# Optimization experiments

Measured on AMD Instinct MI355X. Metric: run time of the kernel, lower is better.

The kernel has to match this reference:

```python
import jax, jax.numpy as jnp
import numpy as np
from jax import lax


def setup_inputs() -> dict:
    key = jax.random.key(0)
    k = jax.random.split(key, 5)
    B, L, ntaps, C = 128, 16384, 128, 128
    return {
        "x": jax.random.normal(k[0], (B, 1, L), dtype=jnp.float32),
        "conv_w": jax.random.normal(k[1], (C, 1, 3), dtype=jnp.float32) * 0.1,
        "conv_b": jax.random.normal(k[2], (C,), dtype=jnp.float32) * 0.1,
        "fc_w": jax.random.normal(k[3], (ntaps, C), dtype=jnp.float32) * 0.05,
        "fc_b": jax.random.normal(k[4], (ntaps,), dtype=jnp.float32) * 0.05,
        "ntaps": ntaps,
    }


def reference(x, conv_w, conv_b, fc_w, fc_b, ntaps):
    # ---- Localiser: Conv1d(1,128,3,padding=1) -> AdaptiveAvgPool1d(1) -> Linear(128, ntaps)
    h = lax.conv_general_dilated(
        x, conv_w, window_strides=(1,), padding=[(1, 1)],
        dimension_numbers=("NCH", "OIH", "NCH"))  # [B,128,L]
    h = h + conv_b[None, :, None]
    pooled = jnp.mean(h, axis=2)                  # [B,128]
    filt = pooled @ fc_w.T + fc_b                 # [B,ntaps]

    # ---- adaptive_filter: per-sample conv1d via groups=B, padding=ntaps
    B = x.shape[0]
    xr = jnp.transpose(x, (1, 0, 2))              # [1,B,L] (batch as channels)
    w = filt[:, None, :]                          # [B,1,ntaps]
    y = lax.conv_general_dilated(
        xr, w, window_strides=(1,), padding=[(ntaps, ntaps)],
        dimension_numbers=("NCH", "OIH", "NCH"),
        feature_group_count=B)                    # [1,B,L+ntaps+1]
    return jnp.transpose(y, (1, 0, 2))            # [B,1,L+ntaps+1]
```

## Files before the change

### kernel.cpp

```cpp
#include <hip/hip_runtime.h>

#define LEN   16384
#define NB    128
#define NTAPS 128
#define LOUT  16513
#define NT    33
#define SPAN  (NT*256 + 144)

typedef __attribute__((ext_vector_type(8))) short bf16x8;
typedef __attribute__((ext_vector_type(4))) float f32x4;

__device__ __forceinline__ unsigned short f2bf(float f) {
    union { float f; unsigned u; } c; c.f = f;
    unsigned r = c.u + 0x7FFF + ((c.u >> 16) & 1);
    return (unsigned short)(r >> 16);
}

__global__ __launch_bounds__(512) void fused_fir(
    const float* __restrict__ x, const float* __restrict__ conv_w,
    const float* __restrict__ conv_b, const float* __restrict__ fc_w,
    const float* __restrict__ fc_b, float* __restrict__ out)
{
    const int b   = blockIdx.y;
    const int h   = blockIdx.x;
    const int tid = threadIdx.x;

    __shared__ unsigned short sxp[SPAN];
    __shared__ unsigned short fp[288];
    __shared__ float scw[384];
    __shared__ float scb[128];
    __shared__ float sfb[128];
    __shared__ float parts[8];
    __shared__ float sx0, sxl;

    const float* xr  = x + (size_t)b * LEN;
    const float4* xr4 = reinterpret_cast<const float4*>(xr);

    if (tid < 384) scw[tid] = conv_w[tid];
    else if (tid < 512) scb[tid - 384] = conv_b[tid - 384];
    if (tid < 128) sfb[tid] = fc_b[tid];
    if (tid == 0) { sx0 = xr[0]; sxl = xr[LEN - 1]; }

    float s = 0.f;
    const int sbase = 32 - 2112 * h;
    #pragma unroll
    for (int p = 0; p < 8; ++p) {
        const int g4 = tid + p * 512;
        float4 v = xr4[g4];
        s += (v.x + v.y) + (v.z + v.w);
        const int s4 = g4 + sbase;
        if (s4 >= 0 && s4 < SPAN / 4) {
            ushort4 hv;
            hv.x = f2bf(v.x); hv.y = f2bf(v.y); hv.z = f2bf(v.z); hv.w = f2bf(v.w);
            *reinterpret_cast<ushort4*>(&sxp[4 * s4]) = hv;
        }
    }
    {
        const ushort4 z = {0, 0, 0, 0};
        if (h == 0) {
            if (tid < 32) *reinterpret_cast<ushort4*>(&sxp[4 * tid]) = z;
        } else {
            if (tid < 132) *reinterpret_cast<ushort4*>(&sxp[4 * (2016 + tid)]) = z;
        }
    }

    const int t = tid >> 2, q = tid & 3;
    const float4* fw4 = reinterpret_cast<const float4*>(fc_w);
    float4 fw[8];
    #pragma unroll
    for (int m = 0; m < 8; ++m) fw[m] = fw4[8 * tid + m];

    #pragma unroll
    for (int off = 32; off > 0; off >>= 1) s += __shfl_down(s, off, 64);
    if ((tid & 63) == 0) parts[tid >> 6] = s;
    __syncthreads();
    float Sb = 0.f;
    #pragma unroll
    for (int i = 0; i < 8; ++i) Sb += parts[i];

    float g0 = 0.f, g1 = 0.f, g2 = 0.f, hh = 0.f;
    #pragma unroll
    for (int m = 0; m < 8; ++m) {
        const float fv[4] = {fw[m].x, fw[m].y, fw[m].z, fw[m].w};
        #pragma unroll
        for (int jj = 0; jj < 4; ++jj) {
            const int c = 32 * q + 4 * m + jj;
            const float f = fv[jj];
            g0 = fmaf(f, scw[3 * c + 0], g0);
            g1 = fmaf(f, scw[3 * c + 1], g1);
            g2 = fmaf(f, scw[3 * c + 2], g2);
            hh = fmaf(f, scb[c], hh);
        }
    }
    g0 += __shfl_xor(g0, 1); g0 += __shfl_xor(g0, 2);
    g1 += __shfl_xor(g1, 1); g1 += __shfl_xor(g1, 2);
    g2 += __shfl_xor(g2, 1); g2 += __shfl_xor(g2, 2);
    hh += __shfl_xor(hh, 1); hh += __shfl_xor(hh, 2);

    if (q == 0) {
        const float invL = 1.0f / (float)LEN;
        const float flt = sfb[t] + hh
            + invL * fmaf(Sb - sxl, g0, fmaf(Sb, g1, (Sb - sx0) * g2));
        fp[128 + t] = f2bf(flt);
    }
    if (q == 1) fp[t] = 0;
    if (q == 2 && t < 32) fp[256 + t] = 0;
    __syncthreads();

    const int l = tid & 63, w = tid >> 6;
    const int n = l & 15;
    const int g = l >> 4;
    bf16x8 afrag[5];
    #pragma unroll
    for (int kb = 0; kb < 5; ++kb)
        #pragma unroll
        for (int hf = 0; hf < 2; ++hf)
            #pragma unroll
            for (int j = 0; j < 4; ++j)
                afrag[kb][hf * 4 + j] =
                    (short)fp[128 + 32 * kb + 16 * hf + 4 * g + j - n];

    float* orow = out + (size_t)b * LOUT;
    #pragma unroll
    for (int it = 0; it < 5; ++it) {
        const int tau = w + 8 * it;
        if (tau >= NT) break;
        const int T = h * NT + tau;
        if (T >= 65) break;
        const unsigned short* bp = &sxp[tau * 256 + 16 * n + 4 * g];
        f32x4 acc = {0.f, 0.f, 0.f, 0.f};
        #pragma unroll
        for (int kb = 0; kb < 5; ++kb) {
            ushort4 lo = *reinterpret_cast<const ushort4*>(bp + 32 * kb);
            ushort4 hi = *reinterpret_cast<const ushort4*>(bp + 32 * kb + 16);
            bf16x8 bfrag;
            bfrag[0] = (short)lo.x; bfrag[1] = (short)lo.y;
            bfrag[2] = (short)lo.z; bfrag[3] = (short)lo.w;
            bfrag[4] = (short)hi.x; bfrag[5] = (short)hi.y;
            bfrag[6] = (short)hi.z; bfrag[7] = (short)hi.w;
            acc = __builtin_amdgcn_mfma_f32_16x16x32_bf16(afrag[kb], bfrag, acc, 0, 0, 0);
        }
        const int t0 = 256 * T + 16 * n + 4 * g;
        if (T < 64) {
            orow[t0 + 0] = acc[0];
            orow[t0 + 1] = acc[1];
            orow[t0 + 2] = acc[2];
            orow[t0 + 3] = acc[3];
        } else {
            #pragma unroll
            for (int j = 0; j < 4; ++j)
                if (t0 + j < LOUT) orow[t0 + j] = acc[j];
        }
    }
}

extern "C" void kernel_launch(void* const* d_in, const int* in_sizes, int n_in,
                              void* d_out, int out_size, void* d_ws, size_t ws_size,
                              hipStream_t stream)
{
    const float* x      = (const float*)d_in[0];
    const float* conv_w = (const float*)d_in[1];
    const float* conv_b = (const float*)d_in[2];
    const float* fc_w   = (const float*)d_in[3];
    const float* fc_b   = (const float*)d_in[4];
    float* out = (float*)d_out;

    dim3 grid(2, NB);
    fused_fir<<<grid, 512, 0, stream>>>(x, conv_w, conv_b, fc_w, fc_b, out);
}
```

Baseline: 17.99 us.

## Process each batch row in one 1024-thread block and vectorize output stores

Replaces the two 512-thread blocks per batch row with a single 1024-thread block that stages the whole padded row in LDS and computes all 65 output tiles. This stops each half-block from re-reading the full input row just to get the mean, and it lets the zero padding be written inline. Full output tiles are now written with one 16-byte vector store instead of four scalar stores. In exchange the grid drops to 128 blocks, half the previous count, so fewer CUs are busy. The vector stores are also not 16-byte aligned for odd batch rows. A redundant first reduction loop was added, but its results are overwritten and the compiler will likely eliminate it.

```diff
diff --git a/kernel.cpp b/kernel.cpp
--- a/kernel.cpp
+++ b/kernel.cpp
@@ -4,8 +4,8 @@
 #define NB    128
 #define NTAPS 128
 #define LOUT  16513
-#define NT    33
-#define SPAN  (NT*256 + 144)
+#define SPAN  16800
+#define SPAN4 (SPAN/4)
 
 typedef __attribute__((ext_vector_type(8))) short bf16x8;
 typedef __attribute__((ext_vector_type(4))) float f32x4;
@@ -16,13 +16,12 @@
     return (unsigned short)(r >> 16);
 }
 
-__global__ __launch_bounds__(512) void fused_fir(
+__global__ __launch_bounds__(1024) void fused_fir(
     const float* __restrict__ x, const float* __restrict__ conv_w,
     const float* __restrict__ conv_b, const float* __restrict__ fc_w,
     const float* __restrict__ fc_b, float* __restrict__ out)
 {
-    const int b   = blockIdx.y;
-    const int h   = blockIdx.x;
+    const int b   = blockIdx.x;
     const int tid = threadIdx.x;
 
     __shared__ unsigned short sxp[SPAN];
@@ -30,45 +29,37 @@
     __shared__ float scw[384];
     __shared__ float scb[128];
     __shared__ float sfb[128];
-    __shared__ float parts[8];
+    __shared__ float parts[16];
     __shared__ float sx0, sxl;
 
-    const float* xr  = x + (size_t)b * LEN;
+    const float* xr   = x + (size_t)b * LEN;
     const float4* xr4 = reinterpret_cast<const float4*>(xr);
 
     if (tid < 384) scw[tid] = conv_w[tid];
     else if (tid < 512) scb[tid - 384] = conv_b[tid - 384];
-    if (tid < 128) sfb[tid] = fc_b[tid];
+    else if (tid < 640) sfb[tid - 512] = fc_b[tid - 512];
     if (tid == 0) { sx0 = xr[0]; sxl = xr[LEN - 1]; }
 
+    const int t = tid >> 3, q = tid & 7;
+    const float4* fw4 = reinterpret_cast<const float4*>(fc_w);
+    float4 fw[4];
+    #pragma unroll
+    for (int m = 0; m < 4; ++m) fw[m] = fw4[32 * t + 4 * q + m];
+
     float s = 0.f;
-    const int sbase = 32 - 2112 * h;
     #pragma unroll
-    for (int p = 0; p < 8; ++p) {
-        const int g4 = tid + p * 512;
-        float4 v = xr4[g4];
-        s += (v.x + v.y) + (v.z + v.w);
-        const int s4 = g4 + sbase;
-        if (s4 >= 0 && s4 < SPAN / 4) {
+    for (int p = 0; p < 5; ++p) {
+        const int i = tid + 1024 * p;
+        if (i < SPAN4) {
+            const int g4 = i - 32;
+            float4 v = make_float4(0.f, 0.f, 0.f, 0.f);
+            if (g4 >= 0 && g4 < LEN / 4) v = xr4[g4];
+            s += (v.x + v.y) + (v.z + v.w);
             ushort4 hv;
             hv.x = f2bf(v.x); hv.y = f2bf(v.y); hv.z = f2bf(v.z); hv.w = f2bf(v.w);
-            *reinterpret_cast<ushort4*>(&sxp[4 * s4]) = hv;
+            *reinterpret_cast<ushort4*>(&sxp[4 * i]) = hv;
         }
     }
-    {
-        const ushort4 z = {0, 0, 0, 0};
-        if (h == 0) {
-            if (tid < 32) *reinterpret_cast<ushort4*>(&sxp[4 * tid]) = z;
-        } else {
-            if (tid < 132) *reinterpret_cast<ushort4*>(&sxp[4 * (2016 + tid)]) = z;
-        }
-    }
-
-    const int t = tid >> 2, q = tid & 3;
-    const float4* fw4 = reinterpret_cast<const float4*>(fc_w);
-    float4 fw[8];
-    #pragma unroll
-    for (int m = 0; m < 8; ++m) fw[m] = fw4[8 * tid + m];
 
     #pragma unroll
     for (int off = 32; off > 0; off >>= 1) s += __shfl_down(s, off, 64);
@@ -76,15 +67,28 @@
     __syncthreads();
     float Sb = 0.f;
     #pragma unroll
-    for (int i = 0; i < 8; ++i) Sb += parts[i];
+    for (int i = 0; i < 16; ++i) Sb += parts[i];
 
     float g0 = 0.f, g1 = 0.f, g2 = 0.f, hh = 0.f;
     #pragma unroll
-    for (int m = 0; m < 8; ++m) {
+    for (int m = 0; m < 4; ++m) {
         const float fv[4] = {fw[m].x, fw[m].y, fw[m].z, fw[m].w};
         #pragma unroll
         for (int jj = 0; jj < 4; ++jj) {
-            const int c = 32 * q + 4 * m + jj;
+            const int c = 16 * q + 4 * m + jj;
+            const float f = fv[jj];
+            g0 = fmaf(f, scw[3 * c + 0], g0);
+            g1 = fmaf(f, scw[3 * c + 1], g1);
+            g2 = fmaf(f, scb[c], hh) , hh = g2, g2 = 0.f;
+        }
+    }
+    g0 = 0.f; g1 = 0.f; g2 = 0.f; hh = 0.f;
+    #pragma unroll
+    for (int m = 0; m < 4; ++m) {
+        const float fv[4] = {fw[m].x, fw[m].y, fw[m].z, fw[m].w};
+        #pragma unroll
+        for (int jj = 0; jj < 4; ++jj) {
+            const int c = 16 * q + 4 * m + jj;
             const float f = fv[jj];
             g0 = fmaf(f, scw[3 * c + 0], g0);
             g1 = fmaf(f, scw[3 * c + 1], g1);
@@ -92,10 +96,10 @@
             hh = fmaf(f, scb[c], hh);
         }
     }
-    g0 += __shfl_xor(g0, 1); g0 += __shfl_xor(g0, 2);
-    g1 += __shfl_xor(g1, 1); g1 += __shfl_xor(g1, 2);
-    g2 += __shfl_xor(g2, 1); g2 += __shfl_xor(g2, 2);
-    hh += __shfl_xor(hh, 1); hh += __shfl_xor(hh, 2);
+    g0 += __shfl_xor(g0, 1); g0 += __shfl_xor(g0, 2); g0 += __shfl_xor(g0, 4);
+    g1 += __shfl_xor(g1, 1); g1 += __shfl_xor(g1, 2); g1 += __shfl_xor(g1, 4);
+    g2 += __shfl_xor(g2, 1); g2 += __shfl_xor(g2, 2); g2 += __shfl_xor(g2, 4);
+    hh += __shfl_xor(hh, 1); hh += __shfl_xor(hh, 2); hh += __shfl_xor(hh, 4);
 
     if (q == 0) {
         const float invL = 1.0f / (float)LEN;
@@ -123,11 +127,9 @@
     float* orow = out + (size_t)b * LOUT;
     #pragma unroll
     for (int it = 0; it < 5; ++it) {
-        const int tau = w + 8 * it;
-        if (tau >= NT) break;
-        const int T = h * NT + tau;
+        const int T = w + 16 * it;
         if (T >= 65) break;
-        const unsigned short* bp = &sxp[tau * 256 + 16 * n + 4 * g];
+        const unsigned short* bp = &sxp[T * 256 + 16 * n + 4 * g];
         f32x4 acc = {0.f, 0.f, 0.f, 0.f};
         #pragma unroll
         for (int kb = 0; kb < 5; ++kb) {
@@ -142,10 +144,7 @@
         }
         const int t0 = 256 * T + 16 * n + 4 * g;
         if (T < 64) {
-            orow[t0 + 0] = acc[0];
-            orow[t0 + 1] = acc[1];
-            orow[t0 + 2] = acc[2];
-            orow[t0 + 3] = acc[3];
+            *reinterpret_cast<f32x4*>(&orow[t0]) = acc;
         } else {
             #pragma unroll
             for (int j = 0; j < 4; ++j)
@@ -165,6 +164,5 @@
     const float* fc_b   = (const float*)d_in[4];
     float* out = (float*)d_out;
 
-    dim3 grid(2, NB);
-    fused_fir<<<grid, 512, 0, stream>>>(x, conv_w, conv_b, fc_w, fc_b, out);
+    fused_fir<<<dim3(NB), 1024, 0, stream>>>(x, conv_w, conv_b, fc_w, fc_b, out);
 }
```

Result: slower. 21.78 us (+21.1%).

## Split filter into Sb-independent parts to drop a barrier before filter build

Applied to the files above, without the earlier changes.

The per-sample filter is rewritten as A + Sb*B, where A and B do not depend on the block-wide sum of x. Both are built into the MFMA fragments before the reduction result is needed, which removes one __syncthreads between the sum and the filter build. The Sb scaling is applied to the accumulators at the end. Conv weights and biases are now read straight from global memory instead of being staged in LDS, and output stores become 16-byte vector writes. In exchange the MFMA work doubles, since two accumulators are computed. The two-part bf16 split also changes rounding behaviour, and the vector stores land on row addresses not aligned to 16 bytes.

```diff
diff --git a/kernel.cpp b/kernel.cpp
--- a/kernel.cpp
+++ b/kernel.cpp
@@ -1,11 +1,10 @@
 #include <hip/hip_runtime.h>
 
-#define LEN   16384
-#define NB    128
-#define NTAPS 128
-#define LOUT  16513
-#define NT    33
-#define SPAN  (NT*256 + 144)
+#define LEN    16384
+#define NB     128
+#define LOUT   16513
+#define SPAN4  2148
+#define SPAN   (SPAN4*4)
 
 typedef __attribute__((ext_vector_type(8))) short bf16x8;
 typedef __attribute__((ext_vector_type(4))) float f32x4;
@@ -26,30 +25,31 @@
     const int tid = threadIdx.x;
 
     __shared__ unsigned short sxp[SPAN];
-    __shared__ unsigned short fp[288];
-    __shared__ float scw[384];
-    __shared__ float scb[128];
-    __shared__ float sfb[128];
+    __shared__ unsigned short fpA[288];
+    __shared__ unsigned short fpB[288];
     __shared__ float parts[8];
-    __shared__ float sx0, sxl;
 
-    const float* xr  = x + (size_t)b * LEN;
+    const float* xr   = x + (size_t)b * LEN;
     const float4* xr4 = reinterpret_cast<const float4*>(xr);
 
-    if (tid < 384) scw[tid] = conv_w[tid];
-    else if (tid < 512) scb[tid - 384] = conv_b[tid - 384];
-    if (tid < 128) sfb[tid] = fc_b[tid];
-    if (tid == 0) { sx0 = xr[0]; sxl = xr[LEN - 1]; }
+    const float x0 = xr[0];
+    const float xl = xr[LEN - 1];
+
+    const int t = tid >> 2, q = tid & 3;
+    const float4* fw4 = reinterpret_cast<const float4*>(fc_w);
+    float4 fw[8];
+    #pragma unroll
+    for (int m = 0; m < 8; ++m) fw[m] = fw4[32 * t + 8 * q + m];
 
     float s = 0.f;
     const int sbase = 32 - 2112 * h;
     #pragma unroll
     for (int p = 0; p < 8; ++p) {
-        const int g4 = tid + p * 512;
+        const int g4 = tid + 512 * p;
         float4 v = xr4[g4];
         s += (v.x + v.y) + (v.z + v.w);
         const int s4 = g4 + sbase;
-        if (s4 >= 0 && s4 < SPAN / 4) {
+        if (s4 >= 0 && s4 < SPAN4) {
             ushort4 hv;
             hv.x = f2bf(v.x); hv.y = f2bf(v.y); hv.z = f2bf(v.z); hv.w = f2bf(v.w);
             *reinterpret_cast<ushort4*>(&sxp[4 * s4]) = hv;
@@ -57,26 +57,13 @@
     }
     {
         const ushort4 z = {0, 0, 0, 0};
-        if (h == 0) {
-            if (tid < 32) *reinterpret_cast<ushort4*>(&sxp[4 * tid]) = z;
-        } else {
-            if (tid < 132) *reinterpret_cast<ushort4*>(&sxp[4 * (2016 + tid)]) = z;
-        }
+        if (h == 0) { if (tid < 32)  *reinterpret_cast<ushort4*>(&sxp[4 * tid]) = z; }
+        else        { if (tid < 132) *reinterpret_cast<ushort4*>(&sxp[4 * (2016 + tid)]) = z; }
     }
-
-    const int t = tid >> 2, q = tid & 3;
-    const float4* fw4 = reinterpret_cast<const float4*>(fc_w);
-    float4 fw[8];
-    #pragma unroll
-    for (int m = 0; m < 8; ++m) fw[m] = fw4[8 * tid + m];
 
     #pragma unroll
     for (int off = 32; off > 0; off >>= 1) s += __shfl_down(s, off, 64);
     if ((tid & 63) == 0) parts[tid >> 6] = s;
-    __syncthreads();
-    float Sb = 0.f;
-    #pragma unroll
-    for (int i = 0; i < 8; ++i) Sb += parts[i];
 
     float g0 = 0.f, g1 = 0.f, g2 = 0.f, hh = 0.f;
     #pragma unroll
@@ -86,10 +73,10 @@
         for (int jj = 0; jj < 4; ++jj) {
             const int c = 32 * q + 4 * m + jj;
             const float f = fv[jj];
-            g0 = fmaf(f, scw[3 * c + 0], g0);
-            g1 = fmaf(f, scw[3 * c + 1], g1);
-            g2 = fmaf(f, scw[3 * c + 2], g2);
-            hh = fmaf(f, scb[c], hh);
+            g0 = fmaf(f, conv_w[3 * c + 0], g0);
+            g1 = fmaf(f, conv_w[3 * c + 1], g1);
+            g2 = fmaf(f, conv_w[3 * c + 2], g2);
+            hh = fmaf(f, conv_b[c], hh);
         }
     }
     g0 += __shfl_xor(g0, 1); g0 += __shfl_xor(g0, 2);
@@ -99,36 +86,44 @@
 
     if (q == 0) {
         const float invL = 1.0f / (float)LEN;
-        const float flt = sfb[t] + hh
-            + invL * fmaf(Sb - sxl, g0, fmaf(Sb, g1, (Sb - sx0) * g2));
-        fp[128 + t] = f2bf(flt);
+        const float A = fc_b[t] + hh - invL * fmaf(xl, g0, x0 * g2);
+        const float B = invL * ((g0 + g1) + g2);
+        fpA[128 + t] = f2bf(A);
+        fpB[128 + t] = f2bf(B);
     }
-    if (q == 1) fp[t] = 0;
-    if (q == 2 && t < 32) fp[256 + t] = 0;
+    if (q == 1) { fpA[t] = 0; fpB[t] = 0; }
+    if (q == 2 && t < 32) { fpA[256 + t] = 0; fpB[256 + t] = 0; }
+
     __syncthreads();
+
+    float Sb = 0.f;
+    #pragma unroll
+    for (int i = 0; i < 8; ++i) Sb += parts[i];
 
     const int l = tid & 63, w = tid >> 6;
     const int n = l & 15;
     const int g = l >> 4;
-    bf16x8 afrag[5];
+    bf16x8 afA[5], afB[5];
     #pragma unroll
     for (int kb = 0; kb < 5; ++kb)
         #pragma unroll
         for (int hf = 0; hf < 2; ++hf)
             #pragma unroll
-            for (int j = 0; j < 4; ++j)
-                afrag[kb][hf * 4 + j] =
-                    (short)fp[128 + 32 * kb + 16 * hf + 4 * g + j - n];
+            for (int j = 0; j < 4; ++j) {
+                const int idx = 128 + 32 * kb + 16 * hf + 4 * g + j - n;
+                afA[kb][hf * 4 + j] = (short)fpA[idx];
+                afB[kb][hf * 4 + j] = (short)fpB[idx];
+            }
 
     float* orow = out + (size_t)b * LOUT;
     #pragma unroll
     for (int it = 0; it < 5; ++it) {
-        const int tau = w + 8 * it;
-        if (tau >= NT) break;
-        const int T = h * NT + tau;
-        if (T >= 65) break;
-        const unsigned short* bp = &sxp[tau * 256 + 16 * n + 4 * g];
-        f32x4 acc = {0.f, 0.f, 0.f, 0.f};
+        const int T = 33 * h + w + 8 * it;
+        if (T >= 33 + 32 * h) break;
+        const int sT = T - 33 * h;
+        const unsigned short* bp = &sxp[sT * 256 + 16 * n + 4 * g];
+        f32x4 accA = {0.f, 0.f, 0.f, 0.f};
+        f32x4 accB = {0.f, 0.f, 0.f, 0.f};
         #pragma unroll
         for (int kb = 0; kb < 5; ++kb) {
             ushort4 lo = *reinterpret_cast<const ushort4*>(bp + 32 * kb);
@@ -138,18 +133,19 @@
             bfrag[2] = (short)lo.z; bfrag[3] = (short)lo.w;
             bfrag[4] = (short)hi.x; bfrag[5] = (short)hi.y;
             bfrag[6] = (short)hi.z; bfrag[7] = (short)hi.w;
-            acc = __builtin_amdgcn_mfma_f32_16x16x32_bf16(afrag[kb], bfrag, acc, 0, 0, 0);
+            accA = __builtin_amdgcn_mfma_f32_16x16x32_bf16(afA[kb], bfrag, accA, 0, 0, 0);
+            accB = __builtin_amdgcn_mfma_f32_16x16x32_bf16(afB[kb], bfrag, accB, 0, 0, 0);
         }
         const int t0 = 256 * T + 16 * n + 4 * g;
+        f32x4 y;
+        #pragma unroll
+        for (int j = 0; j < 4; ++j) y[j] = fmaf(Sb, accB[j], accA[j]);
         if (T < 64) {
-            orow[t0 + 0] = acc[0];
-            orow[t0 + 1] = acc[1];
-            orow[t0 + 2] = acc[2];
-            orow[t0 + 3] = acc[3];
+            *reinterpret_cast<f32x4*>(&orow[t0]) = y;
         } else {
             #pragma unroll
             for (int j = 0; j < 4; ++j)
-                if (t0 + j < LOUT) orow[t0 + j] = acc[j];
+                if (t0 + j < LOUT) orow[t0 + j] = y[j];
         }
     }
 }
@@ -165,6 +161,5 @@
     const float* fc_b   = (const float*)d_in[4];
     float* out = (float*)d_out;
 
-    dim3 grid(2, NB);
-    fused_fir<<<grid, 512, 0, stream>>>(x, conv_w, conv_b, fc_w, fc_b, out);
+    fused_fir<<<dim3(2, NB), 512, 0, stream>>>(x, conv_w, conv_b, fc_w, fc_b, out);
 }
```

After: 25.59 us. +42.3%, slower.
